# Kernel optimization log

Hardware: AMD Instinct MI355X
Metric: run time of the kernel (lower is better)

## Reference

```python
import jax, jax.numpy as jnp
import numpy as np

EPS = 1e-5  # BatchNorm eps (ME.MinkowskiBatchNorm default)


def setup_inputs() -> dict:
    key = jax.random.key(0)
    k1, k2, k3, k4 = jax.random.split(key, 4)
    N, Cin, Cout, K = 65536, 256, 128, 8  # K = kernel_size**dimension = 2**3
    x = jax.random.normal(k1, (N, Cin), dtype=jnp.float32)
    W = jax.random.normal(k2, (K, Cin, Cout), dtype=jnp.float32) * 0.02
    gamma = jax.random.uniform(k3, (Cout,), dtype=jnp.float32, minval=0.5, maxval=1.5)
    beta = jax.random.normal(k4, (Cout,), dtype=jnp.float32) * 0.1
    return {"x": x, "W": W, "gamma": gamma, "beta": beta}


def reference(x, W, gamma, beta):
    # Transpose Minkowski conv, kernel=2, stride=2, dim=3: each input voxel
    # emits 2^3 = 8 disjoint child voxels; child for offset k gets x @ W[k].
    # Kernel map is identity per offset (no scatter-add collisions because
    # kernel_size == stride), so outputs stack to [8*N, Cout].
    Cout = W.shape[-1]
    out = jnp.einsum('nc,kcd->knd', x, W).reshape(-1, Cout)  # [8N, Cout]
    # MinkowskiBatchNorm over all active output sites (training batch stats).
    mean = jnp.mean(out, axis=0)
    var = jnp.mean(jnp.square(out - mean), axis=0)  # biased var, as BN uses
    y = (out - mean) * jax.lax.rsqrt(var + EPS) * gamma + beta
    return jnp.maximum(y, 0.0)  # MinkowskiReLU
```

## Files before the change

kernel.cpp:

```cpp
#include <hip/hip_runtime.h>
#include <stdint.h>

#define N_ROWS 65536
#define CIN 256
#define COUT 128

typedef __bf16 bf16x8 __attribute__((ext_vector_type(8)));
typedef float f32x4 __attribute__((ext_vector_type(4)));
typedef unsigned short u16;
typedef unsigned int u32;

__device__ __forceinline__ float truncbf(float f) {
  u32 x = __builtin_bit_cast(u32, f) & 0xFFFF0000u;
  return __builtin_bit_cast(float, x);
}
__device__ __forceinline__ u32 packbf(float a, float b) {
  return __builtin_amdgcn_perm(__builtin_bit_cast(u32, b),
                               __builtin_bit_cast(u32, a), 0x07060302u);
}

__device__ __forceinline__ void async_ld16(const void* g, void* l) {
  __builtin_amdgcn_global_load_lds((const __attribute__((address_space(1))) u32*)g,
                                   (__attribute__((address_space(3))) u32*)l,
                                   16, 0, 0);
}

template <bool EMIT_XB>
__global__ __launch_bounds__(512, 2) void gram_partial(const float* __restrict__ x,
                                                       float* __restrict__ part,
                                                       float* __restrict__ csb,
                                                       u32* __restrict__ xb) {
  __shared__ u32 xT[16 * 260];
  __shared__ float cs_s[8][256];
  const int tid = threadIdx.x, lane = tid & 63;
  const int w = tid >> 6;
  const int wm = w >> 2, wn = w & 3;
  const int q = lane >> 4, r = lane & 15;
  const int row0 = blockIdx.x * 256;
  const int cq = tid & 63;
  const int np2 = tid >> 6;

  f32x4 acc[8][4];
  #pragma unroll
  for (int i = 0; i < 8; ++i)
    #pragma unroll
    for (int j = 0; j < 4; ++j) acc[i][j] = (f32x4){0.f, 0.f, 0.f, 0.f};
  f32x4 cs = (f32x4){0.f, 0.f, 0.f, 0.f};

  for (int ch = 0; ch < 8; ++ch) {
    const int r0 = row0 + ch * 32;
    const int nA = r0 + np2 * 2;
    const int nB = r0 + (np2 + 8) * 2;
    f32x4 a0 = *(const f32x4*)&x[(size_t)nA * CIN + 4 * cq];
    f32x4 a1 = *(const f32x4*)&x[(size_t)(nA + 1) * CIN + 4 * cq];
    f32x4 b0 = *(const f32x4*)&x[(size_t)nB * CIN + 4 * cq];
    f32x4 b1 = *(const f32x4*)&x[(size_t)(nB + 1) * CIN + 4 * cq];

    union { u32 d[4]; uint4 v; } pA, pB;
    #pragma unroll
    for (int j = 0; j < 4; ++j) {
      pA.d[j] = packbf(a0[j], a1[j]);
      pB.d[j] = packbf(b0[j], b1[j]);
      cs[j] += truncbf(a0[j]) + truncbf(a1[j]) + truncbf(b0[j]) + truncbf(b1[j]);
    }
    *(uint4*)&xT[np2 * 260 + 4 * cq] = pA.v;
    *(uint4*)&xT[(np2 + 8) * 260 + 4 * cq] = pB.v;
    if (EMIT_XB) {
      uint2 e;
      e.x = packbf(a0[0], a0[1]); e.y = packbf(a0[2], a0[3]);
      *(uint2*)&xb[(size_t)nA * 128 + 2 * cq] = e;
      e.x = packbf(a1[0], a1[1]); e.y = packbf(a1[2], a1[3]);
      *(uint2*)&xb[(size_t)(nA + 1) * 128 + 2 * cq] = e;
      e.x = packbf(b0[0], b0[1]); e.y = packbf(b0[2], b0[3]);
      *(uint2*)&xb[(size_t)nB * 128 + 2 * cq] = e;
      e.x = packbf(b1[0], b1[1]); e.y = packbf(b1[2], b1[3]);
      *(uint2*)&xb[(size_t)(nB + 1) * 128 + 2 * cq] = e;
    }
    __syncthreads();
    bf16x8 af[8], bfr[4];
    #pragma unroll
    for (int mt = 0; mt < 8; ++mt) {
      int c = wm * 128 + mt * 16 + r;
      union { u32 d[4]; bf16x8 v; } t;
      #pragma unroll
      for (int s = 0; s < 4; ++s) t.d[s] = xT[(4 * q + s) * 260 + c];
      af[mt] = t.v;
    }
    #pragma unroll
    for (int nt = 0; nt < 4; ++nt) {
      int c = wn * 64 + nt * 16 + r;
      union { u32 d[4]; bf16x8 v; } t;
      #pragma unroll
      for (int s = 0; s < 4; ++s) t.d[s] = xT[(4 * q + s) * 260 + c];
      bfr[nt] = t.v;
    }
    #pragma unroll
    for (int mt = 0; mt < 8; ++mt)
      #pragma unroll
      for (int nt = 0; nt < 4; ++nt)
        acc[mt][nt] = __builtin_amdgcn_mfma_f32_16x16x32_bf16(af[mt], bfr[nt], acc[mt][nt], 0, 0, 0);
    __syncthreads();
  }

  float* pb = part + (size_t)blockIdx.x * 65536;
  #pragma unroll
  for (int mt = 0; mt < 8; ++mt)
    #pragma unroll
    for (int nt = 0; nt < 4; ++nt)
      #pragma unroll
      for (int i = 0; i < 4; ++i) {
        int row = wm * 128 + mt * 16 + q * 4 + i;
        int col = wn * 64 + nt * 16 + r;
        pb[row * 256 + col] = acc[mt][nt][i];
      }

  *(f32x4*)&cs_s[np2][4 * cq] = cs;
  __syncthreads();
  if (tid < 256) {
    float s = 0.f;
    #pragma unroll
    for (int p = 0; p < 8; ++p) s += cs_s[p][tid];
    csb[(size_t)blockIdx.x * 256 + tid] = s;
  }
}

__global__ __launch_bounds__(256) void gram_reduce(const float* __restrict__ part,
                                                   float* __restrict__ G) {
  __shared__ float red[16][64];
  const int t = threadIdx.x;
  const int fi = t & 15, grp = t >> 4;
  const int g0 = blockIdx.x * 64;
  f32x4 a = (f32x4){0.f, 0.f, 0.f, 0.f};
  const float* p = part + (size_t)(grp * 16) * 65536 + g0 + fi * 4;
  #pragma unroll
  for (int b = 0; b < 16; ++b) a += *(const f32x4*)(p + (size_t)b * 65536);
  *(f32x4*)&red[grp][fi * 4] = a;
  __syncthreads();
  if (t < 64) {
    float s = 0.f;
    #pragma unroll
    for (int gq = 0; gq < 16; ++gq) s += red[gq][t];
    G[g0 + t] = s;
  }
}

__global__ __launch_bounds__(256) void stats_kernel(const float* __restrict__ G,
                                                    const float* __restrict__ csb,
                                                    const float* __restrict__ W,
                                                    const float* __restrict__ gamma,
                                                    const float* __restrict__ beta,
                                                    float* __restrict__ scale,
                                                    float* __restrict__ bias) {
  const int d = blockIdx.x;
  const int t = threadIdx.x;
  __shared__ float wv[256][8];
  __shared__ float rr[16];
  float cst = 0.f;
  for (int b = 0; b < 256; ++b) cst += csb[b * 256 + t];
  float wt[8];
  #pragma unroll
  for (int k = 0; k < 8; ++k) wt[k] = truncbf(W[((size_t)k * CIN + t) * COUT + d]);
  #pragma unroll
  for (int k = 0; k < 8; ++k) wv[t][k] = wt[k];
  __syncthreads();

  float q = 0.f;
  for (int j = 0; j < 256; ++j) {
    float g = G[j * 256 + t];
    float dot = 0.f;
    #pragma unroll
    for (int k = 0; k < 8; ++k) dot += wv[j][k] * wt[k];
    q += g * dot;
  }
  float wsum = 0.f;
  #pragma unroll
  for (int k = 0; k < 8; ++k) wsum += wt[k];
  float m = cst * wsum;

  #pragma unroll
  for (int off = 32; off; off >>= 1) {
    q += __shfl_down(q, off, 64);
    m += __shfl_down(m, off, 64);
  }
  int wid = t >> 6;
  if ((t & 63) == 0) { rr[wid] = q; rr[wid + 8] = m; }
  __syncthreads();
  if (t == 0) {
    float qt = rr[0] + rr[1] + rr[2] + rr[3];
    float mn = rr[8] + rr[9] + rr[10] + rr[11];
    const float invM = 1.f / 524288.f;
    float mean = mn * invM;
    float var = qt * invM - mean * mean;
    float s = gamma[d] * rsqrtf(var + 1e-5f);
    scale[d] = s;
    bias[d] = beta[d] - mean * s;
  }
}

__global__ void wtrans_kernel(const float* __restrict__ W, u16* __restrict__ Wt) {
  __shared__ u16 tile[32][128];
  const int blk = blockIdx.x, t = threadIdx.x;
  const int k = blk >> 3, cb = blk & 7;
  #pragma unroll
  for (int i = 0; i < 4; ++i) {
    int u = t + i * 256;
    int ci = u >> 5, d4 = (u & 31) * 4;
    float4 f = *(const float4*)&W[((size_t)k * CIN + cb * 32 + ci) * COUT + d4];
    uint2 p; p.x = packbf(f.x, f.y); p.y = packbf(f.z, f.w);
    *(uint2*)&tile[ci][d4] = p;
  }
  __syncthreads();
  #pragma unroll
  for (int i = 0; i < 2; ++i) {
    int v = t + i * 256;
    int d = v >> 2, c0 = (v & 3) * 8;
    union { u16 s[8]; uint4 u4; } p;
    #pragma unroll
    for (int j = 0; j < 8; ++j) p.s[j] = tile[c0 + j][d];
    *(uint4*)&Wt[((size_t)blk * 128 + d) * 32 + c0] = p.u4;
  }
}

__global__ __launch_bounds__(256, 2) void gemm_xb(const u16* __restrict__ xb,
                                                  const u16* __restrict__ Wt,
                                                  const float* __restrict__ scale,
                                                  const float* __restrict__ bias,
                                                  float* __restrict__ out) {
  __shared__ u16 As[32768];
  const int tid = threadIdx.x, lane = tid & 63;
  const int w = tid >> 6, wr = w >> 1, wc = w & 1;
  const int q = lane >> 4, r = lane & 15;
  const int m0 = blockIdx.x * 128;

  #pragma unroll
  for (int i = 0; i < 16; ++i) {
    int u = tid + i * 256;
    int cb = u >> 9, row = (u >> 2) & 127;
    int sseg = (u ^ (u >> 3)) & 3;
    const u16* g = xb + (size_t)(m0 + row) * CIN + cb * 32 + sseg * 8;
    async_ld16(g, As + (size_t)u * 8);
  }

  float sv[4], bv[4];
  #pragma unroll
  for (int nt = 0; nt < 4; ++nt) {
    int col = wc * 64 + nt * 16 + r;
    sv[nt] = scale[col]; bv[nt] = bias[col];
  }

  const int boff = (wc * 64 + r) * 32 + q * 8;
  const int sw = (q ^ ((r >> 1) & 3)) * 8;
  bf16x8 bcur[4], bnext[4];
  #pragma unroll
  for (int nt = 0; nt < 4; ++nt)
    bcur[nt] = *(const bf16x8*)&Wt[boff + nt * 512];

  __syncthreads();

  int j = 0;
  for (int k = 0; k < 8; ++k) {
    f32x4 acc[4][4];
    #pragma unroll
    for (int i = 0; i < 4; ++i)
      #pragma unroll
      for (int jj = 0; jj < 4; ++jj) acc[i][jj] = (f32x4){0.f, 0.f, 0.f, 0.f};

    #pragma unroll
    for (int cb = 0; cb < 8; ++cb) {
      if (j < 63) {
        #pragma unroll
        for (int nt = 0; nt < 4; ++nt)
          bnext[nt] = *(const bf16x8*)&Wt[(size_t)(j + 1) * 4096 + boff + nt * 512];
      }
      bf16x8 af[4];
      #pragma unroll
      for (int mt = 0; mt < 4; ++mt)
        af[mt] = *(const bf16x8*)&As[((cb * 128) + wr * 64 + mt * 16 + r) * 32 + sw];
      #pragma unroll
      for (int mt = 0; mt < 4; ++mt)
        #pragma unroll
        for (int nt = 0; nt < 4; ++nt)
          acc[mt][nt] = __builtin_amdgcn_mfma_f32_16x16x32_bf16(af[mt], bcur[nt], acc[mt][nt], 0, 0, 0);
      if (j < 63) {
        #pragma unroll
        for (int nt = 0; nt < 4; ++nt) bcur[nt] = bnext[nt];
      }
      ++j;
    }

    const size_t obase = (size_t)k * N_ROWS + m0;
    #pragma unroll
    for (int mt = 0; mt < 4; ++mt)
      #pragma unroll
      for (int nt = 0; nt < 4; ++nt)
        #pragma unroll
        for (int i = 0; i < 4; ++i) {
          int grow = wr * 64 + mt * 16 + q * 4 + i;
          int col = wc * 64 + nt * 16 + r;
          float y = acc[mt][nt][i] * sv[nt] + bv[nt];
          y = y > 0.f ? y : 0.f;
          out[(obase + grow) * COUT + col] = y;
        }
  }
}

__global__ __launch_bounds__(256, 2) void gemm_fp32(const float* __restrict__ x,
                                                    const u16* __restrict__ Wt,
                                                    const float* __restrict__ scale,
                                                    const float* __restrict__ bias,
                                                    float* __restrict__ out) {
  __shared__ float Asf[4096];
  const int tid = threadIdx.x, lane = tid & 63;
  const int w = tid >> 6, wr = w >> 1, wc = w & 1;
  const int q = lane >> 4, r = lane & 15;
  const int k = blockIdx.x & 7;
  const int m0 = (blockIdx.x >> 3) * 128;

  const u16* wbase = Wt + (size_t)k * 8 * 4096;
  const int boff = (wc * 64 + r) * 32 + q * 8;

  bf16x8 bcur[4], bnext[4];
  #pragma unroll
  for (int nt = 0; nt < 4; ++nt)
    bcur[nt] = *(const bf16x8*)&wbase[boff + nt * 512];

  f32x4 acc[4][4];
  #pragma unroll
  for (int i = 0; i < 4; ++i)
    #pragma unroll
    for (int j = 0; j < 4; ++j) acc[i][j] = (f32x4){0.f, 0.f, 0.f, 0.f};

  for (int cb = 0; cb < 8; ++cb) {
    #pragma unroll
    for (int i = 0; i < 4; ++i) {
      int u = tid + i * 256;
      int row = u >> 3;
      int s = (u & 7) ^ (row & 7);
      const float* g = x + (size_t)(m0 + row) * CIN + cb * 32 + s * 4;
      async_ld16(g, Asf + (w * 64 + i * 256) * 4);
    }
    if (cb < 7) {
      #pragma unroll
      for (int nt = 0; nt < 4; ++nt)
        bnext[nt] = *(const bf16x8*)&wbase[(cb + 1) * 4096 + boff + nt * 512];
    }
    __syncthreads();
    bf16x8 af[4];
    #pragma unroll
    for (int mt = 0; mt < 4; ++mt) {
      int row = wr * 64 + mt * 16 + r;
      union { u32 d[4]; bf16x8 v; } t;
      #pragma unroll
      for (int b = 0; b < 2; ++b) {
        int unit = row * 8 + ((2 * q + b) ^ (row & 7));
        float4 f = *(const float4*)&Asf[unit * 4];
        t.d[b * 2 + 0] = packbf(f.x, f.y);
        t.d[b * 2 + 1] = packbf(f.z, f.w);
      }
      af[mt] = t.v;
    }
    #pragma unroll
    for (int mt = 0; mt < 4; ++mt)
      #pragma unroll
      for (int nt = 0; nt < 4; ++nt)
        acc[mt][nt] = __builtin_amdgcn_mfma_f32_16x16x32_bf16(af[mt], bcur[nt], acc[mt][nt], 0, 0, 0);
    __syncthreads();
    if (cb < 7) {
      #pragma unroll
      for (int nt = 0; nt < 4; ++nt) bcur[nt] = bnext[nt];
    }
  }

  float sv[4], bv[4];
  #pragma unroll
  for (int nt = 0; nt < 4; ++nt) {
    int col = wc * 64 + nt * 16 + r;
    sv[nt] = scale[col]; bv[nt] = bias[col];
  }
  const size_t obase = (size_t)k * N_ROWS + m0;
  #pragma unroll
  for (int mt = 0; mt < 4; ++mt)
    #pragma unroll
    for (int nt = 0; nt < 4; ++nt)
      #pragma unroll
      for (int i = 0; i < 4; ++i) {
        int grow = wr * 64 + mt * 16 + q * 4 + i;
        int col = wc * 64 + nt * 16 + r;
        float y = acc[mt][nt][i] * sv[nt] + bv[nt];
        y = y > 0.f ? y : 0.f;
        out[(obase + grow) * COUT + col] = y;
      }
}

extern "C" void kernel_launch(void* const* d_in, const int* in_sizes, int n_in,
                              void* d_out, int out_size, void* d_ws, size_t ws_size,
                              hipStream_t stream) {
  const float* x = (const float*)d_in[0];
  const float* W = (const float*)d_in[1];
  const float* gamma = (const float*)d_in[2];
  const float* beta = (const float*)d_in[3];
  float* out = (float*)d_out;

  float* ws = (float*)d_ws;
  float* G = ws;
  float* csb = ws + 65536;
  float* scale = ws + 131072;
  float* bias = ws + 131200;
  u16* Wt = (u16*)(ws + 131328);
  u32* xb = (u32*)((char*)d_ws + (2u << 20));
  const size_t need = (2u << 20) + (size_t)N_ROWS * CIN * 2;
  const bool big_ws = ws_size >= need;

  float* part = (float*)d_out;

  if (big_ws) {
    gram_partial<true><<<256, 512, 0, stream>>>(x, part, csb, xb);
  } else {
    gram_partial<false><<<256, 512, 0, stream>>>(x, part, csb, xb);
  }
  gram_reduce<<<1024, 256, 0, stream>>>(part, G);
  stats_kernel<<<128, 256, 0, stream>>>(G, csb, W, gamma, beta, scale, bias);
  wtrans_kernel<<<64, 256, 0, stream>>>(W, Wt);
  if (big_ws) {
    gemm_xb<<<512, 256, 0, stream>>>((const u16*)xb, Wt, scale, bias, out);
  } else {
    gemm_fp32<<<4096, 256, 0, stream>>>(x, Wt, scale, bias, out);
  }
}
```

Baseline: 398.4 us.

## Store Gram partials as bf16, prefetch x rows, fuse weight transpose into gram kernel

Gram partial sums are packed to bf16 pairs with round-to-nearest-even before being written, which halves the partial-buffer write and the matching read in the reduce kernel; the reduce kernel is reworked to unpack and sum both halves. The x loads for the next chunk are software-prefetched ahead of the MFMA phase. The separate weight-transpose launch is folded into the first 64 blocks of gram_partial. Rounding the partials to bf16 adds error to the Gram matrix, and therefore to the BN variance estimate, which could affect accuracy.

Result: faster. 383.2 us (-3.8%).

```diff
diff --git a/kernel.cpp b/kernel.cpp
--- a/kernel.cpp
+++ b/kernel.cpp
@@ -18,6 +18,11 @@
   return __builtin_amdgcn_perm(__builtin_bit_cast(u32, b),
                                __builtin_bit_cast(u32, a), 0x07060302u);
 }
+__device__ __forceinline__ u32 bf_rne(float f) {
+  u32 u = __builtin_bit_cast(u32, f);
+  u += 0x7FFFu + ((u >> 16) & 1);
+  return u >> 16;
+}
 
 __device__ __forceinline__ void async_ld16(const void* g, void* l) {
   __builtin_amdgcn_global_load_lds((const __attribute__((address_space(1))) u32*)g,
@@ -27,11 +32,14 @@
 
 template <bool EMIT_XB>
 __global__ __launch_bounds__(512, 2) void gram_partial(const float* __restrict__ x,
-                                                       float* __restrict__ part,
+                                                       u32* __restrict__ part,
                                                        float* __restrict__ csb,
-                                                       u32* __restrict__ xb) {
+                                                       u32* __restrict__ xb,
+                                                       const float* __restrict__ W,
+                                                       u16* __restrict__ Wt) {
   __shared__ u32 xT[16 * 260];
   __shared__ float cs_s[8][256];
+  __shared__ u16 tile[32][128];
   const int tid = threadIdx.x, lane = tid & 63;
   const int w = tid >> 6;
   const int wm = w >> 2, wn = w & 3;
@@ -47,14 +55,20 @@
     for (int j = 0; j < 4; ++j) acc[i][j] = (f32x4){0.f, 0.f, 0.f, 0.f};
   f32x4 cs = (f32x4){0.f, 0.f, 0.f, 0.f};
 
+  f32x4 a0, a1, b0, b1;
+  {
+    const int nA = row0 + np2 * 2;
+    const int nB = row0 + (np2 + 8) * 2;
+    a0 = *(const f32x4*)&x[(size_t)nA * CIN + 4 * cq];
+    a1 = *(const f32x4*)&x[(size_t)(nA + 1) * CIN + 4 * cq];
+    b0 = *(const f32x4*)&x[(size_t)nB * CIN + 4 * cq];
+    b1 = *(const f32x4*)&x[(size_t)(nB + 1) * CIN + 4 * cq];
+  }
+
   for (int ch = 0; ch < 8; ++ch) {
     const int r0 = row0 + ch * 32;
     const int nA = r0 + np2 * 2;
     const int nB = r0 + (np2 + 8) * 2;
-    f32x4 a0 = *(const f32x4*)&x[(size_t)nA * CIN + 4 * cq];
-    f32x4 a1 = *(const f32x4*)&x[(size_t)(nA + 1) * CIN + 4 * cq];
-    f32x4 b0 = *(const f32x4*)&x[(size_t)nB * CIN + 4 * cq];
-    f32x4 b1 = *(const f32x4*)&x[(size_t)(nB + 1) * CIN + 4 * cq];
 
     union { u32 d[4]; uint4 v; } pA, pB;
     #pragma unroll
@@ -76,6 +90,14 @@
       e.x = packbf(b1[0], b1[1]); e.y = packbf(b1[2], b1[3]);
       *(uint2*)&xb[(size_t)(nB + 1) * 128 + 2 * cq] = e;
     }
+    f32x4 na0, na1, nb0, nb1;
+    if (ch < 7) {
+      const int mA = nA + 32, mB = nB + 32;
+      na0 = *(const f32x4*)&x[(size_t)mA * CIN + 4 * cq];
+      na1 = *(const f32x4*)&x[(size_t)(mA + 1) * CIN + 4 * cq];
+      nb0 = *(const f32x4*)&x[(size_t)mB * CIN + 4 * cq];
+      nb1 = *(const f32x4*)&x[(size_t)(mB + 1) * CIN + 4 * cq];
+    }
     __syncthreads();
     bf16x8 af[8], bfr[4];
     #pragma unroll
@@ -100,19 +122,19 @@
       for (int nt = 0; nt < 4; ++nt)
         acc[mt][nt] = __builtin_amdgcn_mfma_f32_16x16x32_bf16(af[mt], bfr[nt], acc[mt][nt], 0, 0, 0);
     __syncthreads();
-  }
-
-  float* pb = part + (size_t)blockIdx.x * 65536;
+    if (ch < 7) { a0 = na0; a1 = na1; b0 = nb0; b1 = nb1; }
+  }
+
+  u32* pb = part + (size_t)blockIdx.x * 32768;
   #pragma unroll
   for (int mt = 0; mt < 8; ++mt)
     #pragma unroll
-    for (int nt = 0; nt < 4; ++nt)
-      #pragma unroll
-      for (int i = 0; i < 4; ++i) {
-        int row = wm * 128 + mt * 16 + q * 4 + i;
-        int col = wn * 64 + nt * 16 + r;
-        pb[row * 256 + col] = acc[mt][nt][i];
-      }
+    for (int nt = 0; nt < 4; ++nt) {
+      int prow = wm * 64 + mt * 8 + q * 2;
+      int col = wn * 64 + nt * 16 + r;
+      pb[prow * 256 + col] = (bf_rne(acc[mt][nt][1]) << 16) | bf_rne(acc[mt][nt][0]);
+      pb[(prow + 1) * 256 + col] = (bf_rne(acc[mt][nt][3]) << 16) | bf_rne(acc[mt][nt][2]);
+    }
 
   *(f32x4*)&cs_s[np2][4 * cq] = cs;
   __syncthreads();
@@ -122,25 +144,59 @@
     for (int p = 0; p < 8; ++p) s += cs_s[p][tid];
     csb[(size_t)blockIdx.x * 256 + tid] = s;
   }
-}
-
-__global__ __launch_bounds__(256) void gram_reduce(const float* __restrict__ part,
+
+  if (blockIdx.x < 64) {
+    const int k = blockIdx.x >> 3, cb = blockIdx.x & 7;
+    #pragma unroll
+    for (int i = 0; i < 2; ++i) {
+      int u = tid + i * 512;
+      int ci = u >> 5, d4 = (u & 31) * 4;
+      float4 f = *(const float4*)&W[((size_t)k * CIN + cb * 32 + ci) * COUT + d4];
+      uint2 p; p.x = packbf(f.x, f.y); p.y = packbf(f.z, f.w);
+      *(uint2*)&tile[ci][d4] = p;
+    }
+    __syncthreads();
+    {
+      int d = tid >> 2, c0 = (tid & 3) * 8;
+      union { u16 s[8]; uint4 u4; } p;
+      #pragma unroll
+      for (int j = 0; j < 8; ++j) p.s[j] = tile[c0 + j][d];
+      *(uint4*)&Wt[((size_t)blockIdx.x * 128 + d) * 32 + c0] = p.u4;
+    }
+  }
+}
+
+__global__ __launch_bounds__(256) void gram_reduce(const u32* __restrict__ part,
                                                    float* __restrict__ G) {
-  __shared__ float red[16][64];
+  __shared__ float red[16][128];
   const int t = threadIdx.x;
   const int fi = t & 15, grp = t >> 4;
   const int g0 = blockIdx.x * 64;
-  f32x4 a = (f32x4){0.f, 0.f, 0.f, 0.f};
-  const float* p = part + (size_t)(grp * 16) * 65536 + g0 + fi * 4;
-  #pragma unroll
-  for (int b = 0; b < 16; ++b) a += *(const f32x4*)(p + (size_t)b * 65536);
-  *(f32x4*)&red[grp][fi * 4] = a;
+  const int rp = g0 >> 8, c0 = g0 & 255;
+  float fa[4] = {0.f, 0.f, 0.f, 0.f}, fb[4] = {0.f, 0.f, 0.f, 0.f};
+  const u32* p = part + (size_t)(grp * 16) * 32768 + g0 + fi * 4;
+  #pragma unroll
+  for (int b = 0; b < 16; ++b) {
+    uint4 u = *(const uint4*)(p + (size_t)b * 32768);
+    const u32* uu = (const u32*)&u;
+    #pragma unroll
+    for (int j = 0; j < 4; ++j) {
+      fa[j] += __builtin_bit_cast(float, uu[j] << 16);
+      fb[j] += __builtin_bit_cast(float, uu[j] & 0xFFFF0000u);
+    }
+  }
+  #pragma unroll
+  for (int j = 0; j < 4; ++j) {
+    float2 v; v.x = fa[j]; v.y = fb[j];
+    *(float2*)&red[grp][(fi * 4 + j) * 2] = v;
+  }
   __syncthreads();
-  if (t < 64) {
+  if (t < 128) {
+    int ci = t & 63, par = t >> 6;
     float s = 0.f;
     #pragma unroll
-    for (int gq = 0; gq < 16; ++gq) s += red[gq][t];
-    G[g0 + t] = s;
+    for (int g = 0; g < 16; ++g) s += red[g][ci * 2 + par];
+    G[(size_t)(2 * rp + par) * 256 + c0 + ci] = s;
   }
 }
 
@@ -197,30 +253,6 @@
   }
 }
 
-__global__ void wtrans_kernel(const float* __restrict__ W, u16* __restrict__ Wt) {
-  __shared__ u16 tile[32][128];
-  const int blk = blockIdx.x, t = threadIdx.x;
-  const int k = blk >> 3, cb = blk & 7;
-  #pragma unroll
-  for (int i = 0; i < 4; ++i) {
-    int u = t + i * 256;
-    int ci = u >> 5, d4 = (u & 31) * 4;
-    float4 f = *(const float4*)&W[((size_t)k * CIN + cb * 32 + ci) * COUT + d4];
-    uint2 p; p.x = packbf(f.x, f.y); p.y = packbf(f.z, f.w);
-    *(uint2*)&tile[ci][d4] = p;
-  }
-  __syncthreads();
-  #pragma unroll
-  for (int i = 0; i < 2; ++i) {
-    int v = t + i * 256;
-    int d = v >> 2, c0 = (v & 3) * 8;
-    union { u16 s[8]; uint4 u4; } p;
-    #pragma unroll
-    for (int j = 0; j < 8; ++j) p.s[j] = tile[c0 + j][d];
-    *(uint4*)&Wt[((size_t)blk * 128 + d) * 32 + c0] = p.u4;
-  }
-}
-
 __global__ __launch_bounds__(256, 2) void gemm_xb(const u16* __restrict__ xb,
                                                   const u16* __restrict__ Wt,
                                                   const float* __restrict__ scale,
@@ -411,16 +443,15 @@
   const size_t need = (2u << 20) + (size_t)N_ROWS * CIN * 2;
   const bool big_ws = ws_size >= need;
 
-  float* part = (float*)d_out;
+  u32* part = (u32*)d_out;
 
   if (big_ws) {
-    gram_partial<true><<<256, 512, 0, stream>>>(x, part, csb, xb);
+    gram_partial<true><<<256, 512, 0, stream>>>(x, part, csb, xb, W, Wt);
   } else {
-    gram_partial<false><<<256, 512, 0, stream>>>(x, part, csb, xb);
-  }
-  gram_reduce<<<1024, 256, 0, stream>>>(part, G);
+    gram_partial<false><<<256, 512, 0, stream>>>(x, part, csb, xb, W, Wt);
+  }
+  gram_reduce<<<512, 256, 0, stream>>>(part, G);
   stats_kernel<<<128, 256, 0, stream>>>(G, csb, W, gamma, beta, scale, bias);
-  wtrans_kernel<<<64, 256, 0, stream>>>(W, Wt);
   if (big_ws) {
     gemm_xb<<<512, 256, 0, stream>>>((const u16*)xb, Wt, scale, bias, out);
   } else {
```
